# Optimization experiments

Hardware: AMD Instinct MI355X
Metric: run time of the kernel (lower is better)

The kernel has to match this reference:

```python
import jax, jax.numpy as jnp
import numpy as np

TOKENS, INPUT, HIDDEN, K = 8192, 1024, 16384, 32

def setup_inputs() -> dict:
    key = jax.random.key(0)
    ks = jax.random.split(key, 6)
    return {
        "x": jax.random.normal(ks[0], (TOKENS, INPUT), dtype=jnp.float32),
        "pre_encode_b": jax.random.normal(ks[1], (INPUT,), dtype=jnp.float32) * 0.1,
        "W": jax.random.normal(ks[2], (HIDDEN, INPUT), dtype=jnp.float32) * 0.01,
        "WT": jax.random.normal(ks[3], (INPUT, HIDDEN), dtype=jnp.float32) * 0.01,
        "b1": jax.random.normal(ks[4], (HIDDEN,), dtype=jnp.float32) * 0.1,
        "b2": jax.random.normal(ks[5], (INPUT,), dtype=jnp.float32) * 0.1,
        "k": K,
    }

def reference(x, pre_encode_b, W, WT, b1, b2, k):
    # encode: dense GEMM [token, hidden]
    xc = x - pre_encode_b
    preacts = jnp.matmul(xc, WT) + b1
    # topk over hidden dim
    vals, idx = jax.lax.top_k(preacts, k)          # [token, k]
    # decode: gather rows of W by topk indices, weighted sum
    Wg = W[idx]                                    # [token, k, input]
    x_hat = jnp.einsum('tk,tki->ti', vals, Wg) + b2
    return x_hat
```

## Files before the change

### kernel.cpp

```cpp
#include <hip/hip_runtime.h>
#include <hip/hip_fp16.h>

#define TOKENS 8192
#define INPUT  1024
#define HIDDEN 16384
#define KSEL   32
#define CANDCAP 96
#define TWO_E  0.006f

typedef __attribute__((ext_vector_type(8))) short bf16x8;
typedef __attribute__((ext_vector_type(4))) float f32x4;

#define GLOAD_LDS16(g, l) __builtin_amdgcn_global_load_lds(              \
    (const __attribute__((address_space(1))) void*)(const void*)(g),     \
    (__attribute__((address_space(3))) void*)(void*)(l), 16, 0, 0)

__device__ inline short f2bf(float f) {
    unsigned u = __float_as_uint(f);
    u += 0x7FFFu + ((u >> 16) & 1u);
    return (short)(u >> 16);
}

__device__ inline float keyToF(unsigned k) {
    unsigned o = (k & 0x8000u) ? (k ^ 0x8000u) : (~k & 0xFFFFu);
    return __half2float(__ushort_as_half((unsigned short)o));
}

__global__ __launch_bounds__(256) void conv_x(
    const float* __restrict__ x, const float* __restrict__ peb,
    short* __restrict__ Abf)
{
    const int g = (blockIdx.x * 256 + threadIdx.x) * 8;
    const int col = g & (INPUT - 1);
    float4 v0 = *(const float4*)&x[g];
    float4 v1 = *(const float4*)&x[g + 4];
    float4 p0 = *(const float4*)&peb[col];
    float4 p1 = *(const float4*)&peb[col + 4];
    short o[8] = {f2bf(v0.x - p0.x), f2bf(v0.y - p0.y), f2bf(v0.z - p0.z), f2bf(v0.w - p0.w),
                  f2bf(v1.x - p1.x), f2bf(v1.y - p1.y), f2bf(v1.z - p1.z), f2bf(v1.w - p1.w)};
    *(bf16x8*)&Abf[g] = *(bf16x8*)o;
}

__global__ __launch_bounds__(256) void transp2(
    const float* __restrict__ WT, float* __restrict__ WTT, short* __restrict__ Btb)
{
    __shared__ float tl[64][65];
    const int bx = blockIdx.x, by = blockIdx.y;
    const int tid = threadIdx.x;
    const int r0 = tid >> 6, c = tid & 63;
#pragma unroll
    for (int i = 0; i < 16; ++i) {
        int r = i * 4 + r0;
        tl[r][c] = WT[(size_t)(by * 64 + r) * HIDDEN + bx * 64 + c];
    }
    __syncthreads();
#pragma unroll
    for (int i = 0; i < 16; ++i) {
        int a = i * 4 + r0;
        float v = tl[c][a];
        size_t o = (size_t)(bx * 64 + a) * INPUT + by * 64 + c;
        WTT[o] = v;
        Btb[o] = f2bf(v);
    }
}

__global__ __launch_bounds__(256) void conv_whf(
    const float* __restrict__ W, unsigned short* __restrict__ Whf)
{
    const size_t g = ((size_t)blockIdx.x * 256 + threadIdx.x) * 8;
    float4 v0 = *(const float4*)&W[g];
    float4 v1 = *(const float4*)&W[g + 4];
    unsigned short o[8] = {
        __half_as_ushort(__float2half(v0.x)), __half_as_ushort(__float2half(v0.y)),
        __half_as_ushort(__float2half(v0.z)), __half_as_ushort(__float2half(v0.w)),
        __half_as_ushort(__float2half(v1.x)), __half_as_ushort(__float2half(v1.y)),
        __half_as_ushort(__float2half(v1.z)), __half_as_ushort(__float2half(v1.w))};
    *(uint4*)&Whf[g] = *(uint4*)o;
}

__global__ __launch_bounds__(512, 2) void gemm_bf16_256(
    const short* __restrict__ A,
    const short* __restrict__ Bt,
    const float* __restrict__ bias1,
    unsigned short* __restrict__ pre16,
    int tok0)
{
    __shared__ short lds[65536];
    const char* L = (const char*)lds;
    const int tid = threadIdx.x;
    const int lane = tid & 63;
    const int w = tid >> 6;
    const int wr = w >> 2, wc = w & 3;

    const int nbx = gridDim.x;
    const int My  = gridDim.y;
    int flat = blockIdx.y * nbx + blockIdx.x;
    const int xcd = flat & 7;
    const int idx = flat >> 3;
    const int colsPerX = nbx >> 3;
    const int q = idx / My;
    const int bm = idx - q * My;
    const int bn = xcd * colsPerX + q;

    const int row0 = tok0 + bm * 256;
    const int col0 = bn * 256;

    const int xr = (lane & 7) << 4;
    const int koff = (lane >> 4) * 16;
    const int swk0 = koff ^ xr;
    const int swk1 = (64 + koff) ^ xr;
    const int aA0 = (wr * 128 + (lane & 15)) * 128 + swk0;
    const int aA1 = (wr * 128 + (lane & 15)) * 128 + swk1;
    const int aB0 = (wc * 64 + (lane & 15)) * 128 + swk0;
    const int aB1 = (wc * 64 + (lane & 15)) * 128 + swk1;

    const int srd = tid >> 3;
    const int scol = ((tid & 7) * 16) ^ ((srd & 7) << 4);
    const short* Asrc = A  + (size_t)(row0 + srd) * INPUT + (scol >> 1);
    const short* Bsrc = Bt + (size_t)(col0 + srd) * INPUT + (scol >> 1);

    f32x4 acc[8][4];
#pragma unroll
    for (int m = 0; m < 8; ++m)
#pragma unroll
        for (int n = 0; n < 4; ++n) acc[m][n] = (f32x4){0.f, 0.f, 0.f, 0.f};

    auto stageA = [&](int slot, int half, int kt) {
        const size_t so = (size_t)(half * 128) * INPUT + kt * 64;
        short* dst = lds + slot * 32768 + half * 8192 + tid * 8;
        GLOAD_LDS16(Asrc + so, dst);
        GLOAD_LDS16(Asrc + so + (size_t)64 * INPUT, dst + 4096);
    };
    auto stageB = [&](int slot, int half, int kt) {
        const size_t so = (size_t)(half * 128) * INPUT + kt * 64;
        short* dst = lds + slot * 32768 + 16384 + half * 8192 + tid * 8;
        GLOAD_LDS16(Bsrc + so, dst);
        GLOAD_LDS16(Bsrc + so + (size_t)64 * INPUT, dst + 4096);
    };

    bf16x8 AQ[8], BL[4], BH[4];

#define RD_A(SAb, mfbase)                                                       \
    _Pragma("unroll") for (int mf = 0; mf < 4; ++mf) {                          \
        AQ[mf * 2 + 0] = *(const bf16x8*)(L + (SAb) + aA0 + ((mfbase) + mf) * 2048); \
        AQ[mf * 2 + 1] = *(const bf16x8*)(L + (SAb) + aA1 + ((mfbase) + mf) * 2048); \
    }
#define RD_B(SBb, BF, nfbase)                                                   \
    _Pragma("unroll") for (int nf = 0; nf < 2; ++nf) {                          \
        BF[nf * 2 + 0] = *(const bf16x8*)(L + (SBb) + aB0 + ((nfbase) + nf) * 2048); \
        BF[nf * 2 + 1] = *(const bf16x8*)(L + (SBb) + aB1 + ((nfbase) + nf) * 2048); \
    }
#define MFMA_Q(BF, mb, nb)                                                      \
    __builtin_amdgcn_s_setprio(1);                                              \
    _Pragma("unroll") for (int mf = 0; mf < 4; ++mf)                            \
        _Pragma("unroll") for (int nf = 0; nf < 2; ++nf)                        \
            _Pragma("unroll") for (int kk = 0; kk < 2; ++kk)                    \
                acc[(mb) + mf][(nb) + nf] = __builtin_amdgcn_mfma_f32_16x16x32_bf16( \
                    AQ[mf * 2 + kk], BF[nf * 2 + kk], acc[(mb) + mf][(nb) + nf], 0, 0, 0); \
    __builtin_amdgcn_s_setprio(0);
#define BAR()  __builtin_amdgcn_s_barrier()
#define LGKM0() asm volatile("s_waitcnt lgkmcnt(0)" ::: "memory")

    stageA(0, 0, 0); stageA(0, 1, 0);
    stageB(0, 0, 0); stageB(0, 1, 0);
    stageB(1, 0, 1); stageB(1, 1, 1);
    asm volatile("s_waitcnt vmcnt(4)" ::: "memory");
    BAR();

    for (int i = 0; i < 8; ++i) {
        const int kt1 = 2 * i + 1, kt2 = 2 * i + 2, kt3 = 2 * i + 3;
        const bool s2 = kt2 < 16, s3 = kt3 < 16;
        RD_A(0, 0); RD_B(32768, BL, 0);
        stageA(1, 0, kt1);
        BAR(); LGKM0();
        MFMA_Q(BL, 0, 0);
        BAR();
        RD_B(32768, BH, 2);
        stageA(1, 1, kt1);
        BAR(); LGKM0();
        MFMA_Q(BH, 0, 2);
        BAR();
        RD_A(0, 4);
        if (s2) stageB(0, 0, kt2);
        BAR(); LGKM0();
        MFMA_Q(BL, 4, 0);
        BAR();
        if (s2) stageB(0, 1, kt2);
        BAR(); LGKM0();
        MFMA_Q(BH, 4, 2);
        if (i < 7) { asm volatile("s_waitcnt vmcnt(4)" ::: "memory"); }
        else       { asm volatile("s_waitcnt vmcnt(0)" ::: "memory"); }
        BAR();
        RD_A(65536, 0); RD_B(98304, BL, 0);
        if (s2) stageA(0, 0, kt2);
        BAR(); LGKM0();
        MFMA_Q(BL, 0, 0);
        BAR();
        RD_B(98304, BH, 2);
        if (s2) stageA(0, 1, kt2);
        BAR(); LGKM0();
        MFMA_Q(BH, 0, 2);
        BAR();
        RD_A(65536, 4);
        if (s3) stageB(1, 0, kt3);
        BAR(); LGKM0();
        MFMA_Q(BL, 4, 0);
        BAR();
        if (s3) stageB(1, 1, kt3);
        BAR(); LGKM0();
        MFMA_Q(BH, 4, 2);
        if (i < 7) { asm volatile("s_waitcnt vmcnt(4)" ::: "memory"); }
        BAR();
    }
#undef RD_A
#undef RD_B
#undef MFMA_Q
#undef BAR
#undef LGKM0

    __syncthreads();

    float bb[4];
#pragma unroll
    for (int nf = 0; nf < 4; ++nf)
        bb[nf] = bias1[col0 + wc * 64 + nf * 16 + (lane & 15)];

    unsigned short* LE = (unsigned short*)lds;
#pragma unroll
    for (int g4 = 0; g4 < 2; ++g4) {
#pragma unroll
        for (int m4 = 0; m4 < 4; ++m4) {
            const int mf = g4 * 4 + m4;
#pragma unroll
            for (int nf = 0; nf < 4; ++nf) {
#pragma unroll
                for (int r = 0; r < 4; ++r) {
                    int er = m4 * 32 + wr * 16 + (lane >> 4) * 4 + r;
                    int ec = wc * 64 + nf * 16 + (lane & 15);
                    LE[er * 264 + ec] = __half_as_ushort(__float2half(acc[mf][nf][r] + bb[nf]));
                }
            }
        }
        __syncthreads();
#pragma unroll
        for (int rd = 0; rd < 8; ++rd) {
            int idx2 = rd * 512 + tid;
            int el = idx2 >> 5;
            int c8 = (idx2 & 31) * 8;
            int m4 = el >> 5;
            int er = el & 31;
            int b  = er >> 4;
            int grow = bm * 256 + b * 128 + (g4 * 4 + m4) * 16 + (er & 15);
            uint4 v = *(const uint4*)&LE[el * 264 + c8];
            *(uint4*)&pre16[(size_t)grow * HIDDEN + col0 + c8] = v;
        }
        __syncthreads();
    }
}

__global__ __launch_bounds__(256) void topcand3(
    const unsigned short* __restrict__ pre16,
    int* __restrict__ cand, float* __restrict__ scr,
    int* __restrict__ ncand, int tok0)
{
    const int tid = threadIdx.x;
    const int t = blockIdx.x;
    const unsigned short* row = pre16 + (size_t)t * HIDDEN;

    unsigned pk[32];
#pragma unroll
    for (int i = 0; i < 8; ++i) {
        uint4 raw = *(const uint4*)&row[(size_t)tid * 64 + i * 8];
        unsigned rr[4] = {raw.x, raw.y, raw.z, raw.w};
#pragma unroll
        for (int j = 0; j < 4; ++j) {
            unsigned lo16 = rr[j] & 0xFFFFu, hi16 = rr[j] >> 16;
            lo16 ^= (((lo16 >> 15) * 0xFFFFu) | 0x8000u);
            hi16 ^= (((hi16 >> 15) * 0xFFFFu) | 0x8000u);
            pk[i * 4 + j] = lo16 | (hi16 << 16);
        }
    }

    __shared__ unsigned wsum[4];
    const int lane = tid & 63, wid = tid >> 6;

    auto countGE = [&](unsigned tau) -> unsigned {
        unsigned c = 0;
#pragma unroll
        for (int i = 0; i < 32; ++i) {
            c += ((pk[i] & 0xFFFFu) >= tau) ? 1u : 0u;
            c += ((pk[i] >> 16) >= tau) ? 1u : 0u;
        }
#pragma unroll
        for (int s = 32; s > 0; s >>= 1) c += __shfl_xor(c, s, 64);
        if (lane == 0) wsum[wid] = c;
        __syncthreads();
        unsigned tot = wsum[0] + wsum[1] + wsum[2] + wsum[3];
        __syncthreads();
        return tot;
    };

    unsigned lo = 0, hi = 0xFFFFu;
    for (int it = 0; it < 17 && lo < hi; ++it) {
        unsigned mid = (lo + hi + 1) >> 1;
        unsigned c = countGE(mid);
        if (c >= 40u) { lo = mid; if (c <= 48u) break; }
        else hi = mid - 1;
    }
    float v40 = keyToF(lo);
    float vthr = v40 - (TWO_E + 0.002f);
    unsigned kthr = (unsigned)__half_as_ushort(__float2half(vthr));
    kthr ^= (((kthr >> 15) * 0xFFFFu) | 0x8000u);

    unsigned mycnt = 0;
#pragma unroll
    for (int i = 0; i < 32; ++i) {
        mycnt += ((pk[i] & 0xFFFFu) >= kthr) ? 1u : 0u;
        mycnt += ((pk[i] >> 16) >= kthr) ? 1u : 0u;
    }
    unsigned inc = mycnt;
#pragma unroll
    for (int s = 1; s < 64; s <<= 1) {
        unsigned o = __shfl_up(inc, s, 64);
        if (lane >= s) inc += o;
    }
    __shared__ unsigned wtot[4];
    if (lane == 63) wtot[wid] = inc;
    __syncthreads();
    unsigned base = inc - mycnt;
    for (int k = 0; k < wid; ++k) base += wtot[k];
    unsigned tot = wtot[0] + wtot[1] + wtot[2] + wtot[3];

    const int gtok = tok0 + t;
    unsigned pos = base;
#pragma unroll
    for (int i = 0; i < 32; ++i) {
        unsigned l16 = pk[i] & 0xFFFFu, h16 = pk[i] >> 16;
        if (l16 >= kthr) {
            if (pos < CANDCAP) {
                cand[(size_t)gtok * CANDCAP + pos] = tid * 64 + i * 2;
                scr[(size_t)gtok * CANDCAP + pos] = keyToF(l16);
            }
            ++pos;
        }
        if (h16 >= kthr) {
            if (pos < CANDCAP) {
                cand[(size_t)gtok * CANDCAP + pos] = tid * 64 + i * 2 + 1;
                scr[(size_t)gtok * CANDCAP + pos] = keyToF(h16);
            }
            ++pos;
        }
    }
    if (tid == 0) ncand[gtok] = (int)(tot < (unsigned)CANDCAP ? tot : (unsigned)CANDCAP);
}

__global__ __launch_bounds__(256) void rescore_select_wave(
    const float* __restrict__ x, const float* __restrict__ peb,
    const float* __restrict__ WTT, const float* __restrict__ bias1,
    const int* __restrict__ cand, const float* __restrict__ scr,
    const int* __restrict__ ncand,
    float* __restrict__ selv, int* __restrict__ seli)
{
    const int wid = threadIdx.x >> 6, lane = threadIdx.x & 63;
    const int t = blockIdx.x * 4 + wid;

    __shared__ double bexL[4][CANDCAP];
    __shared__ short bandL[4][CANDCAP];

    double xc[16];
#pragma unroll
    for (int st = 0; st < 16; ++st) {
        int j = lane + st * 64;
        xc[st] = (double)x[(size_t)t * INPUT + j] - (double)peb[j];
    }

    const int nc0 = ncand[t];
    const int nc = nc0 < CANDCAP ? nc0 : CANDCAP;

    float sv0 = 0.f, sv1 = 0.f;
    int si0 = 0, si1 = 0;
    const bool a0 = lane < nc, a1 = (64 + lane) < nc;
    if (a0) { sv0 = scr[(size_t)t * CANDCAP + lane]; si0 = cand[(size_t)t * CANDCAP + lane]; }
    if (a1) { sv1 = scr[(size_t)t * CANDCAP + 64 + lane]; si1 = cand[(size_t)t * CANDCAP + 64 + lane]; }

    int r0 = 0, r1 = 0;
    for (int k = 0; k < nc; ++k) {
        float vk; int hk;
        if (k < 64) { vk = __shfl(sv0, k, 64); hk = __shfl(si0, k, 64); }
        else        { vk = __shfl(sv1, k - 64, 64); hk = __shfl(si1, k - 64, 64); }
        if (a0 && (vk > sv0 || (vk == sv0 && hk < si0))) ++r0;
        if (a1 && (vk > sv1 || (vk == sv1 && hk < si1))) ++r1;
    }

    unsigned long long b31_0 = __ballot(a0 && r0 == 31);
    unsigned long long b31_1 = __ballot(a1 && r1 == 31);
    float s32;
    if (b31_0) s32 = __shfl(sv0, (int)__ffsll((long long)b31_0) - 1, 64);
    else       s32 = __shfl(sv1, (int)__ffsll((long long)b31_1) - 1, 64);

    const int f0 = a0 ? ((sv0 > s32 + TWO_E) ? 2 : ((sv0 >= s32 - TWO_E) ? 1 : 0)) : 0;
    const int f1 = a1 ? ((sv1 > s32 + TWO_E) ? 2 : ((sv1 >= s32 - TWO_E) ? 1 : 0)) : 0;

    const unsigned long long mi0 = __ballot(f0 == 2), mi1 = __ballot(f1 == 2);
    const unsigned long long mb0 = __ballot(f0 == 1), mb1 = __ballot(f1 == 1);
    const int nin = __popcll(mi0) + __popcll(mi1);
    const int bn = __popcll(mb0) + __popcll(mb1);
    const int need = KSEL - nin;

    const unsigned long long ltmask = (lane == 63) ? 0x7FFFFFFFFFFFFFFFull
                                                   : ((1ull << lane) - 1ull);
    if (f0 == 1) bandL[wid][__popcll(mb0 & ltmask)] = (short)lane;
    if (f1 == 1) bandL[wid][__popcll(mb0) + __popcll(mb1 & ltmask)] = (short)(64 + lane);

    for (int jb = 0; jb < bn; ++jb) {
        const int c = bandL[wid][jb];
        const int h = (c < 64) ? __shfl(si0, c, 64) : __shfl(si1, c - 64, 64);
        const float* wrow = WTT + (size_t)h * INPUT;
        double s = 0.0;
#pragma unroll
        for (int st = 0; st < 16; ++st)
            s += (double)wrow[lane + st * 64] * xc[st];
#pragma unroll
        for (int off = 32; off > 0; off >>= 1)
            s += __shfl_xor(s, off, 64);
        if (lane == 0) bexL[wid][c] = s + (double)bias1[h];
    }

    int s0 = 0, s1 = 0;
    {
        double v0 = 0.0, v1 = 0.0;
        if (f0 == 1) v0 = bexL[wid][lane];
        if (f1 == 1) v1 = bexL[wid][64 + lane];
        int rb0 = 0, rb1 = 0;
        for (int k = 0; k < bn; ++k) {
            const int ck = bandL[wid][k];
            const int hk = (ck < 64) ? __shfl(si0, ck, 64) : __shfl(si1, ck - 64, 64);
            const double vk = bexL[wid][ck];
            if (f0 == 1 && (vk > v0 || (vk == v0 && hk < si0))) ++rb0;
            if (f1 == 1 && (vk > v1 || (vk == v1 && hk < si1))) ++rb1;
        }
        if (f0 == 2 || (f0 == 1 && rb0 < need)) s0 = 1;
        if (f1 == 2 || (f1 == 1 && rb1 < need)) s1 = 1;

        const unsigned long long ms0 = __ballot(s0), ms1 = __ballot(s1);
        if (s0) {
            int pos = __popcll(ms0 & ltmask);
            if (pos < KSEL) {
                selv[(size_t)t * KSEL + pos] = (f0 == 2) ? sv0 : (float)v0;
                seli[(size_t)t * KSEL + pos] = si0;
            }
        }
        if (s1) {
            int pos = __popcll(ms0) + __popcll(ms1 & ltmask);
            if (pos < KSEL) {
                selv[(size_t)t * KSEL + pos] = (f1 == 2) ? sv1 : (float)v1;
                seli[(size_t)t * KSEL + pos] = si1;
            }
        }
    }
}

__global__ __launch_bounds__(512) void decode512(
    const float* __restrict__ selv, const int* __restrict__ seli,
    const unsigned short* __restrict__ Whf, const float* __restrict__ b2,
    float* __restrict__ out)
{
    const int t = blockIdx.x;
    const int tid = threadIdx.x;
    const int jh = tid >> 8;
    const int cpos = tid & 255;
    const int c = cpos * 4;
    __shared__ float sv[KSEL];
    __shared__ int si[KSEL];
    __shared__ float4 red[256];
    if (tid < KSEL) {
        sv[tid] = selv[(size_t)t * KSEL + tid];
        si[tid] = seli[(size_t)t * KSEL + tid];
    }
    __syncthreads();
    float4 acc = {0.f, 0.f, 0.f, 0.f};
    const int j0 = jh * 16;
#pragma unroll 8
    for (int j = j0; j < j0 + 16; ++j) {
        uint2 raw = *(const uint2*)&Whf[(size_t)si[j] * INPUT + c];
        const float s = sv[j];
        float2 f0 = __half22float2(*(__half2*)&raw.x);
        float2 f1 = __half22float2(*(__half2*)&raw.y);
        acc.x += s * f0.x; acc.y += s * f0.y; acc.z += s * f1.x; acc.w += s * f1.y;
    }
    if (jh == 1) red[cpos] = acc;
    __syncthreads();
    if (jh == 0) {
        float4 o = red[cpos];
        float4 bb = *(const float4*)&b2[c];
        o.x += acc.x + bb.x; o.y += acc.y + bb.y;
        o.z += acc.z + bb.z; o.w += acc.w + bb.w;
        *(float4*)&out[(size_t)t * INPUT + c] = o;
    }
}

extern "C" void kernel_launch(void* const* d_in, const int* in_sizes, int n_in,
                              void* d_out, int out_size, void* d_ws, size_t ws_size,
                              hipStream_t stream) {
    const float* x   = (const float*)d_in[0];
    const float* peb = (const float*)d_in[1];
    const float* W   = (const float*)d_in[2];
    const float* WT  = (const float*)d_in[3];
    const float* b1  = (const float*)d_in[4];
    const float* b2  = (const float*)d_in[5];
    float* out = (float*)d_out;

    char* p = (char*)d_ws;
    int*   candb = (int*)p;            p += (size_t)TOKENS * CANDCAP * 4;
    float* scrb  = (float*)p;          p += (size_t)TOKENS * CANDCAP * 4;
    int*   ncb   = (int*)p;            p += (size_t)TOKENS * 4;
    float* selvb = (float*)p;          p += (size_t)TOKENS * KSEL * 4;
    int*   selib = (int*)p;            p += (size_t)TOKENS * KSEL * 4;
    float* WTT   = (float*)p;          p += (size_t)HIDDEN * INPUT * 4;
    short* Abf   = (short*)p;          p += (size_t)TOKENS * INPUT * 2;
    short* Btb   = (short*)p;          p += (size_t)HIDDEN * INPUT * 2;
    unsigned short* Whf = (unsigned short*)p; p += (size_t)HIDDEN * INPUT * 2;
    unsigned short* pre16 = (unsigned short*)p;

    size_t used = (size_t)(p - (char*)d_ws);
    size_t avail = ws_size > used ? ws_size - used : 0;
    long cap = (long)(avail / ((size_t)HIDDEN * 2));
    cap = (cap / 256) * 256;
    if (cap > TOKENS) cap = TOKENS;
    if (cap < 256) cap = 256;

    conv_x<<<dim3(TOKENS * INPUT / (256 * 8)), dim3(256), 0, stream>>>(x, peb, Abf);
    transp2<<<dim3(HIDDEN / 64, INPUT / 64), dim3(256), 0, stream>>>(WT, WTT, Btb);
    conv_whf<<<dim3((unsigned)((size_t)HIDDEN * INPUT / (256 * 8))), dim3(256), 0, stream>>>(W, Whf);

    for (int tok0 = 0; tok0 < TOKENS; tok0 += (int)cap) {
        int M = TOKENS - tok0;
        if (M > cap) M = (int)cap;
        gemm_bf16_256<<<dim3(HIDDEN / 256, M / 256), dim3(512), 0, stream>>>(
            Abf, Btb, b1, pre16, tok0);
        topcand3<<<dim3(M), dim3(256), 0, stream>>>(pre16, candb, scrb, ncb, tok0);
    }

    rescore_select_wave<<<dim3(TOKENS / 4), dim3(256), 0, stream>>>(
        x, peb, WTT, b1, candb, scrb, ncb, selvb, selib);
    decode512<<<dim3(TOKENS), dim3(512), 0, stream>>>(selvb, selib, Whf, b2, out);
}
```

Measured before the change: 609.8 us.

## Emit per-tile row maxima in GEMM epilogue to prune top-k candidate scanning

```diff
diff --git a/kernel.cpp b/kernel.cpp
--- a/kernel.cpp
+++ b/kernel.cpp
@@ -83,6 +83,7 @@
     const short* __restrict__ Bt,
     const float* __restrict__ bias1,
     unsigned short* __restrict__ pre16,
+    unsigned short* __restrict__ tmax,
     int tok0)
 {
     __shared__ short lds[65536];
@@ -254,36 +255,85 @@
             uint4 v = *(const uint4*)&LE[el * 264 + c8];
             *(uint4*)&pre16[(size_t)grow * HIDDEN + col0 + c8] = v;
         }
+        {
+            const int el = tid >> 2, qq = tid & 3;
+            const unsigned short* rowp = &LE[el * 264 + qq * 64];
+            float m = -3.0e38f;
+#pragma unroll
+            for (int i8 = 0; i8 < 8; ++i8) {
+                uint4 rv = *(const uint4*)&rowp[i8 * 8];
+                unsigned rr4[4] = {rv.x, rv.y, rv.z, rv.w};
+#pragma unroll
+                for (int jj = 0; jj < 4; ++jj) {
+                    m = fmaxf(m, __half2float(__ushort_as_half((unsigned short)(rr4[jj] & 0xFFFFu))));
+                    m = fmaxf(m, __half2float(__ushort_as_half((unsigned short)(rr4[jj] >> 16))));
+                }
+            }
+            m = fmaxf(m, __shfl_xor(m, 1, 64));
+            m = fmaxf(m, __shfl_xor(m, 2, 64));
+            if (qq == 0) {
+                int m4 = el >> 5, er5 = el & 31, bsub = er5 >> 4, rrow = er5 & 15;
+                int grow = bm * 256 + bsub * 128 + (g4 * 4 + m4) * 16 + rrow;
+                tmax[(size_t)grow * 64 + bn] = __half_as_ushort(__float2half(m));
+            }
+        }
         __syncthreads();
     }
 }
 
 __global__ __launch_bounds__(256) void topcand3(
     const unsigned short* __restrict__ pre16,
+    const unsigned short* __restrict__ tmax,
     int* __restrict__ cand, float* __restrict__ scr,
     int* __restrict__ ncand, int tok0)
 {
     const int tid = threadIdx.x;
     const int t = blockIdx.x;
     const unsigned short* row = pre16 + (size_t)t * HIDDEN;
+    const int lane = tid & 63, wid = tid >> 6;
+
+    __shared__ unsigned short tkeys[64];
+    __shared__ unsigned tauLB_s;
+    if (tid < 64) {
+        unsigned u = tmax[(size_t)t * 64 + tid];
+        u ^= (((u >> 15) * 0xFFFFu) | 0x8000u);
+        tkeys[tid] = (unsigned short)u;
+        int rk = 0;
+        for (int k = 0; k < 64; ++k) {
+            unsigned ok = __shfl(u, k, 64);
+            if (ok > u || (ok == u && k < tid)) ++rk;
+        }
+        if (rk == 39) {
+            float lb = keyToF(u) - 0.010f;
+            unsigned kk = (unsigned)__half_as_ushort(__float2half(lb));
+            kk ^= (((kk >> 15) * 0xFFFFu) | 0x8000u);
+            tauLB_s = kk;
+        }
+    }
+    __syncthreads();
+    const unsigned tauLB = tauLB_s;
+    const bool live = ((unsigned)tkeys[tid >> 2]) >= tauLB;
 
     unsigned pk[32];
-#pragma unroll
-    for (int i = 0; i < 8; ++i) {
-        uint4 raw = *(const uint4*)&row[(size_t)tid * 64 + i * 8];
-        unsigned rr[4] = {raw.x, raw.y, raw.z, raw.w};
-#pragma unroll
-        for (int j = 0; j < 4; ++j) {
-            unsigned lo16 = rr[j] & 0xFFFFu, hi16 = rr[j] >> 16;
-            lo16 ^= (((lo16 >> 15) * 0xFFFFu) | 0x8000u);
-            hi16 ^= (((hi16 >> 15) * 0xFFFFu) | 0x8000u);
-            pk[i * 4 + j] = lo16 | (hi16 << 16);
-        }
+    if (live) {
+#pragma unroll
+        for (int i = 0; i < 8; ++i) {
+            uint4 raw = *(const uint4*)&row[(size_t)tid * 64 + i * 8];
+            unsigned rr[4] = {raw.x, raw.y, raw.z, raw.w};
+#pragma unroll
+            for (int j = 0; j < 4; ++j) {
+                unsigned lo16 = rr[j] & 0xFFFFu, hi16 = rr[j] >> 16;
+                lo16 ^= (((lo16 >> 15) * 0xFFFFu) | 0x8000u);
+                hi16 ^= (((hi16 >> 15) * 0xFFFFu) | 0x8000u);
+                pk[i * 4 + j] = lo16 | (hi16 << 16);
+            }
+        }
+    } else {
+#pragma unroll
+        for (int i = 0; i < 32; ++i) pk[i] = 0;
     }
 
     __shared__ unsigned wsum[4];
-    const int lane = tid & 63, wid = tid >> 6;
-
     auto countGE = [&](unsigned tau) -> unsigned {
         unsigned c = 0;
 #pragma unroll
@@ -300,7 +350,7 @@
         return tot;
     };
 
-    unsigned lo = 0, hi = 0xFFFFu;
+    unsigned lo = tauLB, hi = 0xFFFFu;
     for (int it = 0; it < 17 && lo < hi; ++it) {
         unsigned mid = (lo + hi + 1) >> 1;
         unsigned c = countGE(mid);
@@ -516,6 +566,7 @@
     int*   ncb   = (int*)p;            p += (size_t)TOKENS * 4;
     float* selvb = (float*)p;          p += (size_t)TOKENS * KSEL * 4;
     int*   selib = (int*)p;            p += (size_t)TOKENS * KSEL * 4;
+    unsigned short* tmaxb = (unsigned short*)p; p += (size_t)TOKENS * 64 * 2;
     float* WTT   = (float*)p;          p += (size_t)HIDDEN * INPUT * 4;
     short* Abf   = (short*)p;          p += (size_t)TOKENS * INPUT * 2;
     short* Btb   = (short*)p;          p += (size_t)HIDDEN * INPUT * 2;
@@ -537,8 +588,8 @@
         int M = TOKENS - tok0;
         if (M > cap) M = (int)cap;
         gemm_bf16_256<<<dim3(HIDDEN / 256, M / 256), dim3(512), 0, stream>>>(
-            Abf, Btb, b1, pre16, tok0);
-        topcand3<<<dim3(M), dim3(256), 0, stream>>>(pre16, candb, scrb, ncb, tok0);
+            Abf, Btb, b1, pre16, tmaxb, tok0);
+        topcand3<<<dim3(M), dim3(256), 0, stream>>>(pre16, tmaxb, candb, scrb, ncb, tok0);
     }
 
     rescore_select_wave<<<dim3(TOKENS / 4), dim3(256), 0, stream>>>(
```

New measurement: 650.7 us. 1.07x slower.
